# Performance work log

Hardware: AMD Instinct MI355X
Metric: run time of the kernel (lower is better)

## Reference

```python
import jax, jax.numpy as jnp
import numpy as np

N = 50000      # nodes
E = 800000     # edges (avg degree 16)
D_IN, D_H, D_OUT = 128, 128, 64
EPS = 1e-5


def setup_inputs() -> dict:
    key = jax.random.key(0)
    ks = jax.random.split(key, 6)
    feat = jax.random.normal(ks[0], (N, D_IN), dtype=jnp.float32)
    # Consistent CSR adjacency: sorted destination rows -> nodePointer via searchsorted
    rows = np.sort(np.asarray(jax.random.randint(ks[1], (E,), 0, N, dtype=jnp.int32)))
    edge_rows = jnp.asarray(rows, dtype=jnp.int32)              # [E] destination node per edge
    nodePointer = jnp.asarray(np.searchsorted(rows, np.arange(N + 1)), dtype=jnp.int32)  # [N+1]
    edgeList = jax.random.randint(ks[2], (E,), 0, N, dtype=jnp.int32)  # [E] source (column) indices
    def glorot(k, i, o):
        return jax.random.normal(k, (i, o), dtype=jnp.float32) * (1.0 / np.sqrt(i)).astype(np.float32)
    W0 = glorot(ks[3], D_IN, D_H)
    W1 = glorot(ks[4], D_H, D_H)
    W2 = glorot(ks[5], D_H, D_OUT)
    return {"feat": feat, "W0": W0, "W1": W1, "W2": W2,
            "nodePointer": nodePointer, "edgeList": edgeList, "edge_rows": edge_rows}


def _layer_norm(x):
    # Fresh nn.LayerNorm each forward in the original => weight=1, bias=0
    mu = jnp.mean(x, axis=-1, keepdims=True)
    var = jnp.mean(jnp.square(x - mu), axis=-1, keepdims=True)
    return (x - mu) * jax.lax.rsqrt(var + EPS)


def reference(feat, W0, W1, W2, nodePointer, edgeList, edge_rows):
    h = feat
    Ws = [W0, W1, W2]
    n_layers = len(Ws)
    for l, W in enumerate(Ws):
        xw = h @ W                      # [N, d_out] dense GEMM
        msg = xw[edgeList]              # [E, d_out] gather source-node features
        h = jax.ops.segment_sum(msg, edge_rows, num_segments=N)  # SpMM: A @ (h W)
        h = _layer_norm(h)
        if l != n_layers - 1:
            h = jax.nn.relu(h)
    return h
```

## Files before the change

kernel.cpp:

```cpp
#include <hip/hip_runtime.h>
#include <cstddef>


typedef __attribute__((ext_vector_type(8))) short bf16x8;
typedef __attribute__((ext_vector_type(4))) float floatx4;
typedef __attribute__((ext_vector_type(4))) unsigned int uintx4;
typedef __attribute__((ext_vector_type(2))) unsigned int uintx2;

static __device__ __forceinline__ unsigned int f2bf(float f) {
    union { float f; unsigned int u; } v; v.f = f;
    unsigned int u = v.u;
    u += 0x7fffu + ((u >> 16) & 1u);
    return u >> 16;
}
static __device__ __forceinline__ float bf_lo(unsigned int p) {
    union { unsigned int u; float f; } v; v.u = p << 16; return v.f;
}
static __device__ __forceinline__ float bf_hi(unsigned int p) {
    union { unsigned int u; float f; } v; v.u = p & 0xffff0000u; return v.f;
}
static __device__ __forceinline__ void acc8(float* a, uintx4 v) {
    a[0] += bf_lo(v.x); a[1] += bf_hi(v.x);
    a[2] += bf_lo(v.y); a[3] += bf_hi(v.y);
    a[4] += bf_lo(v.z); a[5] += bf_hi(v.z);
    a[6] += bf_lo(v.w); a[7] += bf_hi(v.w);
}
static __device__ __forceinline__ void acc4(float* a, uintx2 v) {
    a[0] += bf_lo(v.x); a[1] += bf_hi(v.x);
    a[2] += bf_lo(v.y); a[3] += bf_hi(v.y);
}

__global__ __launch_bounds__(256) void cvt_w(const float* __restrict__ W0,
                                             const float* __restrict__ W1,
                                             const float* __restrict__ W2,
                                             unsigned int* __restrict__ Wt) {
    const int m = blockIdx.x >> 4;
    const int slice = blockIdx.x & 15;
    const float* W = (m == 0) ? W0 : (m == 1) ? W1 : W2;
    const int ncols = (m == 2) ? 64 : 128;
    unsigned int* dst = Wt + m * 128 * 64;
    const int total = ncols * 64;
    for (int idx = slice * 256 + threadIdx.x; idx < total; idx += 16 * 256) {
        int kk = idx / ncols;
        int n  = idx - kk * ncols;
        unsigned int lo = f2bf(W[(size_t)(2 * kk) * ncols + n]);
        unsigned int hi = f2bf(W[(size_t)(2 * kk + 1) * ncols + n]);
        dst[(size_t)n * 64 + kk] = (hi << 16) | lo;
    }
}

template <int NCOLS, bool A_FP32>
__global__ __launch_bounds__(64) void gemm_mfma(const void* __restrict__ Av,
                                                const unsigned int* __restrict__ Wt,
                                                unsigned int* __restrict__ C,
                                                int M) {
    const int lane = threadIdx.x;
    const int row0 = blockIdx.x * 16;
    const int quad = lane >> 4;
    const int mcol = lane & 15;
    int aidx = row0 + mcol; if (aidx >= M) aidx = M - 1;

    constexpr int NT = NCOLS / 16;
    floatx4 acc[NT];
    #pragma unroll
    for (int t = 0; t < NT; ++t) acc[t] = (floatx4){0.f, 0.f, 0.f, 0.f};

    const float*        arowF = (const float*)Av + (size_t)aidx * 128 + quad * 8;
    const unsigned int* arowB = (const unsigned int*)Av + (size_t)aidx * 64 + quad * 4;

    #pragma unroll
    for (int k0 = 0; k0 < 128; k0 += 32) {
        bf16x8 a;
        if constexpr (A_FP32) {
            float4 fa = *(const float4*)(arowF + k0);
            float4 fb = *(const float4*)(arowF + k0 + 4);
            uintx4 ap;
            ap.x = (f2bf(fa.y) << 16) | f2bf(fa.x);
            ap.y = (f2bf(fa.w) << 16) | f2bf(fa.z);
            ap.z = (f2bf(fb.y) << 16) | f2bf(fb.x);
            ap.w = (f2bf(fb.w) << 16) | f2bf(fb.z);
            a = __builtin_bit_cast(bf16x8, ap);
        } else {
            uintx4 ap = *(const uintx4*)(arowB + k0 / 2);
            a = __builtin_bit_cast(bf16x8, ap);
        }

        const int koff = (k0 + quad * 8) >> 1;
        #pragma unroll
        for (int t = 0; t < NT; ++t) {
            const unsigned int* brow = Wt + (size_t)(t * 16 + mcol) * 64 + koff;
            uintx4 bp = *(const uintx4*)brow;
            bf16x8 b = __builtin_bit_cast(bf16x8, bp);
            acc[t] = __builtin_amdgcn_mfma_f32_16x16x32_bf16(a, b, acc[t], 0, 0, 0);
        }
    }

    const int rowStride = NCOLS >> 1;
    #pragma unroll
    for (int t = 0; t < NT; ++t) {
        #pragma unroll
        for (int r = 0; r < 4; ++r) {
            unsigned int mybf = f2bf(acc[t][r]);
            unsigned int pair = __shfl_xor(mybf, 1, 64);
            int orow = row0 + quad * 4 + r;
            if (orow < M && (mcol & 1) == 0) {
                unsigned int packed = (pair << 16) | mybf;
                C[(size_t)orow * rowStride + t * 8 + (mcol >> 1)] = packed;
            }
        }
    }
}

__global__ __launch_bounds__(256) void agg_ln128(const unsigned int* __restrict__ xw,
                                                 const int* __restrict__ ptr,
                                                 const int* __restrict__ col,
                                                 unsigned int* __restrict__ out,
                                                 int N) {
    const int node = blockIdx.x * 4 + (threadIdx.x >> 6);
    if (node >= N) return;
    const int lane = threadIdx.x & 63;
    const int g  = lane >> 4;
    const int sl = lane & 15;
    const int s = ptr[node];
    const int e = ptr[node + 1];

    float accA[8] = {}, accB[8] = {};
    const unsigned int* base = xw + sl * 4;
    int i = s + g;
    for (; i + 12 < e; i += 16) {
        uintx4 v0 = *(const uintx4*)(base + (size_t)col[i]      * 64);
        uintx4 v1 = *(const uintx4*)(base + (size_t)col[i + 4]  * 64);
        uintx4 v2 = *(const uintx4*)(base + (size_t)col[i + 8]  * 64);
        uintx4 v3 = *(const uintx4*)(base + (size_t)col[i + 12] * 64);
        acc8(accA, v0); acc8(accB, v1); acc8(accA, v2); acc8(accB, v3);
    }
    for (; i < e; i += 4) {
        uintx4 v0 = *(const uintx4*)(base + (size_t)col[i] * 64);
        acc8(accA, v0);
    }

    float acc[8];
    #pragma unroll
    for (int j = 0; j < 8; ++j) acc[j] = accA[j] + accB[j];

    #pragma unroll
    for (int j = 0; j < 8; ++j) {
        acc[j] += __shfl_xor(acc[j], 16, 64);
        acc[j] += __shfl_xor(acc[j], 32, 64);
    }
    float s1 = 0.f, s2 = 0.f;
    #pragma unroll
    for (int j = 0; j < 8; ++j) { s1 += acc[j]; s2 += acc[j] * acc[j]; }
    #pragma unroll
    for (int m = 8; m >= 1; m >>= 1) {
        s1 += __shfl_xor(s1, m, 64);
        s2 += __shfl_xor(s2, m, 64);
    }
    const float mean = s1 * (1.0f / 128.0f);
    const float var  = s2 * (1.0f / 128.0f) - mean * mean;
    const float inv  = rsqrtf(var + 1e-5f);

    if (g == 0) {
        float o[8];
        #pragma unroll
        for (int j = 0; j < 8; ++j)
            o[j] = fmaxf((acc[j] - mean) * inv, 0.f);
        uintx4 p;
        p.x = (f2bf(o[1]) << 16) | f2bf(o[0]);
        p.y = (f2bf(o[3]) << 16) | f2bf(o[2]);
        p.z = (f2bf(o[5]) << 16) | f2bf(o[4]);
        p.w = (f2bf(o[7]) << 16) | f2bf(o[6]);
        *(uintx4*)(out + (size_t)node * 64 + sl * 4) = p;
    }
}

__global__ __launch_bounds__(256) void agg_ln64(const unsigned int* __restrict__ xw,
                                                const int* __restrict__ ptr,
                                                const int* __restrict__ col,
                                                float* __restrict__ out, int N) {
    const int node = blockIdx.x * 4 + (threadIdx.x >> 6);
    if (node >= N) return;
    const int lane = threadIdx.x & 63;
    const int g  = lane >> 4;
    const int sl = lane & 15;
    const int s = ptr[node];
    const int e = ptr[node + 1];

    float accA[4] = {}, accB[4] = {};
    const unsigned int* base = xw + sl * 2;
    int i = s + g;
    for (; i + 12 < e; i += 16) {
        uintx2 v0 = *(const uintx2*)(base + (size_t)col[i]      * 32);
        uintx2 v1 = *(const uintx2*)(base + (size_t)col[i + 4]  * 32);
        uintx2 v2 = *(const uintx2*)(base + (size_t)col[i + 8]  * 32);
        uintx2 v3 = *(const uintx2*)(base + (size_t)col[i + 12] * 32);
        acc4(accA, v0); acc4(accB, v1); acc4(accA, v2); acc4(accB, v3);
    }
    for (; i < e; i += 4) {
        uintx2 v0 = *(const uintx2*)(base + (size_t)col[i] * 32);
        acc4(accA, v0);
    }

    float acc[4];
    #pragma unroll
    for (int j = 0; j < 4; ++j) acc[j] = accA[j] + accB[j];

    #pragma unroll
    for (int j = 0; j < 4; ++j) {
        acc[j] += __shfl_xor(acc[j], 16, 64);
        acc[j] += __shfl_xor(acc[j], 32, 64);
    }
    float s1 = 0.f, s2 = 0.f;
    #pragma unroll
    for (int j = 0; j < 4; ++j) { s1 += acc[j]; s2 += acc[j] * acc[j]; }
    #pragma unroll
    for (int m = 8; m >= 1; m >>= 1) {
        s1 += __shfl_xor(s1, m, 64);
        s2 += __shfl_xor(s2, m, 64);
    }
    const float mean = s1 * (1.0f / 64.0f);
    const float var  = s2 * (1.0f / 64.0f) - mean * mean;
    const float inv  = rsqrtf(var + 1e-5f);

    if (g == 0) {
        float4 o;
        o.x = (acc[0] - mean) * inv;
        o.y = (acc[1] - mean) * inv;
        o.z = (acc[2] - mean) * inv;
        o.w = (acc[3] - mean) * inv;
        *(float4*)(out + (size_t)node * 64 + sl * 4) = o;
    }
}

extern "C" void kernel_launch(void* const* d_in, const int* in_sizes, int n_in,
                              void* d_out, int out_size, void* d_ws, size_t ws_size,
                              hipStream_t stream) {
    const float* feat = (const float*)d_in[0];
    const float* W0   = (const float*)d_in[1];
    const float* W1   = (const float*)d_in[2];
    const float* W2   = (const float*)d_in[3];
    const int*   ptr  = (const int*)d_in[4];
    const int*   col  = (const int*)d_in[5];

    const int N = in_sizes[4] - 1;

    unsigned int* xwp = (unsigned int*)d_ws;
    unsigned int* hb  = xwp + (size_t)N * 64;
    unsigned int* WtP = hb + (size_t)N * 64;
    float*        out = (float*)d_out;

    const int gemmBlocks = (N + 15) / 16;
    const int nodeBlocks = (N + 3) / 4;

    cvt_w<<<48, 256, 0, stream>>>(W0, W1, W2, WtP);

    gemm_mfma<128, true><<<gemmBlocks, 64, 0, stream>>>(feat, WtP, xwp, N);
    agg_ln128<<<nodeBlocks, 256, 0, stream>>>(xwp, ptr, col, hb, N);
    gemm_mfma<128, false><<<gemmBlocks, 64, 0, stream>>>(hb, WtP + 128 * 64, xwp, N);
    agg_ln128<<<nodeBlocks, 256, 0, stream>>>(xwp, ptr, col, hb, N);
    gemm_mfma<64, false><<<gemmBlocks, 64, 0, stream>>>(hb, WtP + 2 * 128 * 64, xwp, N);
    agg_ln64<<<nodeBlocks, 256, 0, stream>>>(xwp, ptr, col, out, N);
}
```

Baseline: 223.3 us.

## Store weights and hidden activations in MFMA fragment order for coalesced loads

The weight conversion kernel now writes bf16 weights pre-swizzled into the per-lane MFMA B-fragment order. The aggregation+LayerNorm kernel writes its bf16 output in 16-row tiles laid out as MFMA A-fragments. The GEMM then reads both operands with contiguous per-lane 16-byte loads instead of strided row accesses. The tiled output layout requires the node count to be handled in whole 16-row tiles, and the scattered stores in the aggregation kernel may coalesce less well.

New measurement: 201.8 us. 1.11x faster.

```diff
diff --git a/kernel.cpp b/kernel.cpp
--- a/kernel.cpp
+++ b/kernel.cpp
@@ -33,19 +33,25 @@
 __global__ __launch_bounds__(256) void cvt_w(const float* __restrict__ W0,
                                              const float* __restrict__ W1,
                                              const float* __restrict__ W2,
-                                             unsigned int* __restrict__ Wt) {
+                                             unsigned int* __restrict__ WtF) {
     const int m = blockIdx.x >> 4;
     const int slice = blockIdx.x & 15;
     const float* W = (m == 0) ? W0 : (m == 1) ? W1 : W2;
     const int ncols = (m == 2) ? 64 : 128;
-    unsigned int* dst = Wt + m * 128 * 64;
+    unsigned int* dst = WtF + m * 128 * 64;
     const int total = ncols * 64;
     for (int idx = slice * 256 + threadIdx.x; idx < total; idx += 16 * 256) {
-        int kk = idx / ncols;
-        int n  = idx - kk * ncols;
-        unsigned int lo = f2bf(W[(size_t)(2 * kk) * ncols + n]);
-        unsigned int hi = f2bf(W[(size_t)(2 * kk + 1) * ncols + n]);
-        dst[(size_t)n * 64 + kk] = (hi << 16) | lo;
+        const int j    = idx & 3;
+        const int lane = (idx >> 2) & 63;
+        const int s    = (idx >> 8) & 3;
+        const int t    = idx >> 10;
+        const int mcol = lane & 15;
+        const int quad = lane >> 4;
+        const int n = t * 16 + mcol;
+        const int k = s * 32 + quad * 8 + 2 * j;
+        unsigned int lo = f2bf(W[(size_t)k * ncols + n]);
+        unsigned int hi = f2bf(W[(size_t)(k + 1) * ncols + n]);
+        dst[idx] = (hi << 16) | lo;
     }
 }
 
@@ -58,22 +64,23 @@
     const int row0 = blockIdx.x * 16;
     const int quad = lane >> 4;
     const int mcol = lane & 15;
-    int aidx = row0 + mcol; if (aidx >= M) aidx = M - 1;
 
     constexpr int NT = NCOLS / 16;
     floatx4 acc[NT];
     #pragma unroll
     for (int t = 0; t < NT; ++t) acc[t] = (floatx4){0.f, 0.f, 0.f, 0.f};
 
+    int aidx = row0 + mcol; if (aidx >= M) aidx = M - 1;
     const float*        arowF = (const float*)Av + (size_t)aidx * 128 + quad * 8;
-    const unsigned int* arowB = (const unsigned int*)Av + (size_t)aidx * 64 + quad * 4;
-
-    #pragma unroll
-    for (int k0 = 0; k0 < 128; k0 += 32) {
+    const unsigned int* afrag = (const unsigned int*)Av + (size_t)blockIdx.x * 1024 + lane * 4;
+    const unsigned int* bbase = Wt + lane * 4;
+
+    #pragma unroll
+    for (int s = 0; s < 4; ++s) {
         bf16x8 a;
         if constexpr (A_FP32) {
-            float4 fa = *(const float4*)(arowF + k0);
-            float4 fb = *(const float4*)(arowF + k0 + 4);
+            float4 fa = *(const float4*)(arowF + s * 32);
+            float4 fb = *(const float4*)(arowF + s * 32 + 4);
             uintx4 ap;
             ap.x = (f2bf(fa.y) << 16) | f2bf(fa.x);
             ap.y = (f2bf(fa.w) << 16) | f2bf(fa.z);
@@ -81,15 +88,12 @@
             ap.w = (f2bf(fb.w) << 16) | f2bf(fb.z);
             a = __builtin_bit_cast(bf16x8, ap);
         } else {
-            uintx4 ap = *(const uintx4*)(arowB + k0 / 2);
+            uintx4 ap = *(const uintx4*)(afrag + s * 256);
             a = __builtin_bit_cast(bf16x8, ap);
         }
-
-        const int koff = (k0 + quad * 8) >> 1;
         #pragma unroll
         for (int t = 0; t < NT; ++t) {
-            const unsigned int* brow = Wt + (size_t)(t * 16 + mcol) * 64 + koff;
-            uintx4 bp = *(const uintx4*)brow;
+            uintx4 bp = *(const uintx4*)(bbase + t * 1024 + s * 256);
             bf16x8 b = __builtin_bit_cast(bf16x8, bp);
             acc[t] = __builtin_amdgcn_mfma_f32_16x16x32_bf16(a, b, acc[t], 0, 0, 0);
         }
@@ -170,7 +174,8 @@
         p.y = (f2bf(o[3]) << 16) | f2bf(o[2]);
         p.z = (f2bf(o[5]) << 16) | f2bf(o[4]);
         p.w = (f2bf(o[7]) << 16) | f2bf(o[6]);
-        *(uintx4*)(out + (size_t)node * 64 + sl * 4) = p;
+        const int tile = node >> 4, m = node & 15;
+        *(uintx4*)(out + (size_t)tile * 1024 + (sl >> 2) * 256 + (sl & 3) * 64 + m * 4) = p;
     }
 }
 
```
